# Optimization experiments

Hardware: AMD Instinct MI355X
Metric: run time of the kernel (lower is better)

The kernel has to match this reference:

```python
import jax, jax.numpy as jnp
import numpy as np

EPS = 1e-5

def _conv1x1(x, w):
    # x: (B, Cin, N, K), w: (Cout, Cin) -> (B, Cout, N, K)
    return jnp.einsum('oc,bcnk->bonk', w, x)

def _bn2d(x, gamma, beta):
    # eval-mode BN with running_mean=0, running_var=1 (fresh init)
    scale = gamma / jnp.sqrt(1.0 + EPS)
    return x * scale[None, :, None, None] + beta[None, :, None, None]

def setup_inputs() -> dict:
    key = jax.random.key(0)
    ks = jax.random.split(key, 10)
    B, Cin, N, K = 8, 64, 1024, 32
    Cout, M = 64, 8
    Cin2 = 2 * Cin  # kernel_input='w_neighbor'
    features = jax.random.normal(ks[0], (B, Cin, N, K), dtype=jnp.float32)
    points_xyz = jax.random.normal(ks[1], (B, 3, N, K), dtype=jnp.float32)
    # ScoreNet convs: mlp_channels [7,16,16,16,M]; first 3 have BN (no bias), last has bias
    w1 = jax.random.normal(ks[2], (16, 7), dtype=jnp.float32) * (2.0 / 7) ** 0.5
    w2 = jax.random.normal(ks[3], (16, 16), dtype=jnp.float32) * (2.0 / 16) ** 0.5
    w3 = jax.random.normal(ks[4], (16, 16), dtype=jnp.float32) * (2.0 / 16) ** 0.5
    w4 = jax.random.normal(ks[5], (M, 16), dtype=jnp.float32) * (2.0 / 16) ** 0.5
    b4 = jnp.zeros((M,), dtype=jnp.float32)
    g1 = jnp.ones((16,), jnp.float32); be1 = jnp.zeros((16,), jnp.float32)
    g2 = jnp.ones((16,), jnp.float32); be2 = jnp.zeros((16,), jnp.float32)
    g3 = jnp.ones((16,), jnp.float32); be3 = jnp.zeros((16,), jnp.float32)
    # weight bank: kaiming_normal on (M, 2Cin, Cout) -> stored as (2Cin, M, Cout)
    wb = jax.random.normal(ks[6], (Cin2, M, Cout), dtype=jnp.float32) * (2.0 / Cin2) ** 0.5
    bn_g = jnp.ones((Cout,), jnp.float32); bn_b = jnp.zeros((Cout,), jnp.float32)
    return dict(features=features, points_xyz=points_xyz,
                w1=w1, g1=g1, be1=be1, w2=w2, g2=g2, be2=be2,
                w3=w3, g3=g3, be3=be3, w4=w4, b4=b4,
                weight_bank=wb, bn_g=bn_g, bn_b=bn_b)

def reference(features, points_xyz, w1, g1, be1, w2, g2, be2, w3, g3, be3,
              w4, b4, weight_bank, bn_g, bn_b):
    B, Cin, N, K = features.shape
    M = weight_bank.shape[1]
    # kernel_input = 'w_neighbor': concat(feat - center, feat) -> (B, 2Cin, N, K)
    center_f = features[..., :1]
    feat = jnp.concatenate([features - center_f, features], axis=1)
    # scorenet input = 'w_neighbor_dist': (center_xyz, xyz_diff, dist) -> (B, 7, N, K)
    center_xyz = jnp.broadcast_to(points_xyz[..., :1], points_xyz.shape)
    xyz_diff = points_xyz - center_xyz
    dist = jnp.sqrt(jnp.sum(xyz_diff * xyz_diff, axis=1, keepdims=True))
    xyz_feats = jnp.concatenate([center_xyz, xyz_diff, dist], axis=1)
    h = jax.nn.relu(_bn2d(_conv1x1(xyz_feats, w1), g1, be1))
    h = jax.nn.relu(_bn2d(_conv1x1(h, w2), g2, be2))
    h = jax.nn.relu(_bn2d(_conv1x1(h, w3), g3, be3))
    s = _conv1x1(h, w4) + b4[None, :, None, None]  # (B, M, N, K)
    scores = jax.nn.softmax(s, axis=1)
    scores = jnp.transpose(scores, (0, 2, 3, 1))  # (B, N, K, M)
    # matmul with weight bank then score-weighted sum over kernels, fused via einsum
    # original: (B,N,K,2Cin)@(2Cin,M*Cout) -> (B,N,K,M,Cout); sum_m scores * . -> (B,N,K,Cout)
    new_features = jnp.einsum('bcnk,cmo,bnkm->bonk', feat, weight_bank, scores)
    # BN2d (eval, fresh stats) + ReLU
    new_features = jax.nn.relu(_bn2d(new_features, bn_g, bn_b))
    return new_features
```

## Files before the change

### kernel.cpp

```cpp
#include <hip/hip_runtime.h>
#include <hip/hip_bf16.h>

typedef _Float16 f16;
typedef __attribute__((ext_vector_type(2))) _Float16 f16x2;
typedef __attribute__((ext_vector_type(8))) _Float16 f16x8;
typedef __attribute__((ext_vector_type(16))) float f32x16;

#define BNSCL 0.9999950000375f

__global__ __launch_bounds__(256) void k_scores(
    const float* __restrict__ xyz,
    const float* __restrict__ w1, const float* __restrict__ g1, const float* __restrict__ be1,
    const float* __restrict__ w2, const float* __restrict__ g2, const float* __restrict__ be2,
    const float* __restrict__ w3, const float* __restrict__ g3, const float* __restrict__ be3,
    const float* __restrict__ w4, const float* __restrict__ b4,
    const float* __restrict__ wb, f16* __restrict__ wbtA,
    f16* __restrict__ scores)
{
    __shared__ float lw[856];
    const int tid = threadIdx.x;

    if (blockIdx.x < 256) {
        int idx = blockIdx.x * 256 + tid;
        int j    = idx & 7;
        int lane = (idx >> 3) & 63;
        int ks   = (idx >> 9) & 63;
        int ot   = idx >> 15;
        int cp   = ks * 2 + (lane >> 5);
        int o    = ot * 32 + (lane & 31);
        wbtA[idx] = (f16)wb[(cp * 8 + j) * 64 + o];
    }

    if (tid < 112) lw[tid] = w1[tid];
    lw[112 + tid] = w2[tid];
    lw[368 + tid] = w3[tid];
    if (tid < 128) lw[624 + tid] = w4[tid];
    if (tid < 8)   lw[752 + tid] = b4[tid];
    if (tid < 16) {
        lw[760 + tid] = g1[tid] * BNSCL;  lw[776 + tid] = be1[tid];
        lw[792 + tid] = g2[tid] * BNSCL;  lw[808 + tid] = be2[tid];
        lw[824 + tid] = g3[tid] * BNSCL;  lw[840 + tid] = be3[tid];
    }
    __syncthreads();

    float in7[2][7], h1[2][16], h2[2][16], s[2][8];

#pragma unroll
    for (int q = 0; q < 2; ++q) {
        int g = blockIdx.x * 512 + q * 256 + tid;
        int b = g >> 15;
        int p = g & 32767;
        int pc = p & ~31;
        const float* xb = xyz + (size_t)b * 98304;
        float cx = xb[pc], cy = xb[32768 + pc], cz = xb[65536 + pc];
        float dx = xb[p] - cx, dy = xb[32768 + p] - cy, dz = xb[65536 + p] - cz;
        in7[q][0] = cx; in7[q][1] = cy; in7[q][2] = cz;
        in7[q][3] = dx; in7[q][4] = dy; in7[q][5] = dz;
        in7[q][6] = sqrtf(dx * dx + dy * dy + dz * dz);
    }

#pragma unroll
    for (int o = 0; o < 16; ++o) {
        float a0 = 0.f, a1 = 0.f;
#pragma unroll
        for (int c = 0; c < 7; ++c) {
            float w = lw[o * 7 + c];
            a0 += w * in7[0][c]; a1 += w * in7[1][c];
        }
        float gs = lw[760 + o], bb = lw[776 + o];
        h1[0][o] = fmaxf(a0 * gs + bb, 0.f);
        h1[1][o] = fmaxf(a1 * gs + bb, 0.f);
    }
#pragma unroll
    for (int o = 0; o < 16; ++o) {
        float a0 = 0.f, a1 = 0.f;
#pragma unroll
        for (int c = 0; c < 16; ++c) {
            float w = lw[112 + o * 16 + c];
            a0 += w * h1[0][c]; a1 += w * h1[1][c];
        }
        float gs = lw[792 + o], bb = lw[808 + o];
        h2[0][o] = fmaxf(a0 * gs + bb, 0.f);
        h2[1][o] = fmaxf(a1 * gs + bb, 0.f);
    }
#pragma unroll
    for (int o = 0; o < 16; ++o) {
        float a0 = 0.f, a1 = 0.f;
#pragma unroll
        for (int c = 0; c < 16; ++c) {
            float w = lw[368 + o * 16 + c];
            a0 += w * h2[0][c]; a1 += w * h2[1][c];
        }
        float gs = lw[824 + o], bb = lw[840 + o];
        h1[0][o] = fmaxf(a0 * gs + bb, 0.f);
        h1[1][o] = fmaxf(a1 * gs + bb, 0.f);
    }
#pragma unroll
    for (int o = 0; o < 8; ++o) {
        float bb = lw[752 + o];
        float a0 = bb, a1 = bb;
#pragma unroll
        for (int c = 0; c < 16; ++c) {
            float w = lw[624 + o * 16 + c];
            a0 += w * h1[0][c]; a1 += w * h1[1][c];
        }
        s[0][o] = a0; s[1][o] = a1;
    }

#pragma unroll
    for (int q = 0; q < 2; ++q) {
        int g = blockIdx.x * 512 + q * 256 + tid;
        float mx = s[q][0];
#pragma unroll
        for (int i = 1; i < 8; ++i) mx = fmaxf(mx, s[q][i]);
        float sum = 0.f;
#pragma unroll
        for (int i = 0; i < 8; ++i) { s[q][i] = __expf(s[q][i] - mx); sum += s[q][i]; }
        float inv = 1.f / sum;
        f16x8 o8;
#pragma unroll
        for (int i = 0; i < 8; ++i) o8[i] = (f16)(s[q][i] * inv);
        *(f16x8*)(scores + (size_t)g * 8) = o8;
    }
}

__global__ __launch_bounds__(512, 4) void k_main(
    const float* __restrict__ feat,
    const f16* __restrict__ scores,
    const f16* __restrict__ wbtA,
    const float* __restrict__ bn_g, const float* __restrict__ bn_b,
    float* __restrict__ out)
{
    __shared__ __align__(16) f16 lwb[32768];

    const int tid  = threadIdx.x;
    const int lane = tid & 63;
    const int wave = tid >> 6;
    const int l31  = lane & 31;
    const int lh   = lane >> 5;

    const int ot = blockIdx.x >> 9;
    const int g  = blockIdx.x & 511;
    const int pblock = g * 512;
    const int b    = pblock >> 15;
    const int pt0  = (pblock & 32767) + wave * 64;
    const int pc0  = pt0 + l31;
    const int pc1  = pc0 + 32;

    const f16* src = wbtA + ((size_t)ot << 15);
#pragma unroll
    for (int it = 0; it < 8; ++it) {
        int idx = it * 512 + tid;
        *(int4*)&lwb[idx << 3] = *(const int4*)&src[idx << 3];
    }
    __syncthreads();

    const float* fb = feat + (size_t)b * 2097152;

    const int gpt = pblock + wave * 64 + l31;
    f16x8 sv0 = *(const f16x8*)(scores + (size_t)gpt * 8);
    f16x8 sv1 = *(const f16x8*)(scores + (size_t)(gpt + 32) * 8);
    const f16x2 s0a = {sv0[0], sv0[1]}, s0b = {sv0[2], sv0[3]},
                s0c = {sv0[4], sv0[5]}, s0d = {sv0[6], sv0[7]};
    const f16x2 s1a = {sv1[0], sv1[1]}, s1b = {sv1[2], sv1[3]},
                s1c = {sv1[4], sv1[5]}, s1d = {sv1[6], sv1[7]};

    f32x16 acc0 = {}, acc1 = {};

    const f16* Alds = lwb + (lane << 3);

#pragma unroll 2
    for (int kk = 0; kk < 32; ++kk) {
        const float* fr = fb + ((size_t)(kk * 2 + lh) << 15);

        f16x8 aD = *(const f16x8*)(Alds + ((size_t)kk << 9));
        f16x8 aR = *(const f16x8*)(Alds + ((size_t)(kk + 32) << 9));

        float fv0 = fr[pc0], fv1 = fr[pc1];
        float fc0 = fr[pt0], fc1 = fr[pt0 + 32];

        f16 hR0 = (f16)fv0,          hR1 = (f16)fv1;
        f16 hD0 = (f16)(fv0 - fc0),  hD1 = (f16)(fv1 - fc1);
        f16x2 fR0 = {hR0, hR0}, fR1 = {hR1, hR1};
        f16x2 fD0 = {hD0, hD0}, fD1 = {hD1, hD1};

        f16x2 d0a = fD0 * s0a, d0b = fD0 * s0b, d0c = fD0 * s0c, d0d = fD0 * s0d;
        f16x2 d1a = fD1 * s1a, d1b = fD1 * s1b, d1c = fD1 * s1c, d1d = fD1 * s1d;
        f16x2 r0a = fR0 * s0a, r0b = fR0 * s0b, r0c = fR0 * s0c, r0d = fR0 * s0d;
        f16x2 r1a = fR1 * s1a, r1b = fR1 * s1b, r1c = fR1 * s1c, r1d = fR1 * s1d;

        f16x8 bD0 = {d0a[0],d0a[1],d0b[0],d0b[1],d0c[0],d0c[1],d0d[0],d0d[1]};
        f16x8 bD1 = {d1a[0],d1a[1],d1b[0],d1b[1],d1c[0],d1c[1],d1d[0],d1d[1]};
        f16x8 bR0 = {r0a[0],r0a[1],r0b[0],r0b[1],r0c[0],r0c[1],r0d[0],r0d[1]};
        f16x8 bR1 = {r1a[0],r1a[1],r1b[0],r1b[1],r1c[0],r1c[1],r1d[0],r1d[1]};

        acc0 = __builtin_amdgcn_mfma_f32_32x32x16_f16(aD, bD0, acc0, 0, 0, 0);
        acc1 = __builtin_amdgcn_mfma_f32_32x32x16_f16(aD, bD1, acc1, 0, 0, 0);
        acc0 = __builtin_amdgcn_mfma_f32_32x32x16_f16(aR, bR0, acc0, 0, 0, 0);
        acc1 = __builtin_amdgcn_mfma_f32_32x32x16_f16(aR, bR1, acc1, 0, 0, 0);
    }

#pragma unroll
    for (int q = 0; q < 2; ++q) {
        int pcol = (q == 0) ? pc0 : pc1;
        const f32x16& a = (q == 0) ? acc0 : acc1;
#pragma unroll
        for (int r = 0; r < 16; ++r) {
            int o = ot * 32 + (r & 3) + ((r >> 2) << 3) + (lh << 2);
            float v = a[r];
            v = v * (bn_g[o] * BNSCL) + bn_b[o];
            v = fmaxf(v, 0.f);
            out[((size_t)(b * 64 + o) << 15) + pcol] = v;
        }
    }
}

extern "C" void kernel_launch(void* const* d_in, const int* in_sizes, int n_in,
                              void* d_out, int out_size, void* d_ws, size_t ws_size,
                              hipStream_t stream)
{
    const float* features = (const float*)d_in[0];
    const float* xyz      = (const float*)d_in[1];
    const float* w1  = (const float*)d_in[2];
    const float* g1  = (const float*)d_in[3];
    const float* be1 = (const float*)d_in[4];
    const float* w2  = (const float*)d_in[5];
    const float* g2  = (const float*)d_in[6];
    const float* be2 = (const float*)d_in[7];
    const float* w3  = (const float*)d_in[8];
    const float* g3  = (const float*)d_in[9];
    const float* be3 = (const float*)d_in[10];
    const float* w4  = (const float*)d_in[11];
    const float* b4  = (const float*)d_in[12];
    const float* wb  = (const float*)d_in[13];
    const float* bn_g = (const float*)d_in[14];
    const float* bn_b = (const float*)d_in[15];

    f16* scores = (f16*)d_ws;
    f16* wbtA   = (f16*)((char*)d_ws + (4u << 20));

    k_scores<<<512, 256, 0, stream>>>(xyz, w1, g1, be1, w2, g2, be2,
                                      w3, g3, be3, w4, b4, wb, wbtA, scores);
    k_main<<<1024, 512, 0, stream>>>(features, scores, wbtA, bn_g, bn_b,
                                     (float*)d_out);
}
```

Baseline: 180.7 us.

## Software-pipeline feature loads four steps ahead and overlap with LDS weight fill

Feature loads for the first four k-steps and the score loads are issued before the shared-memory weight copy and barrier, so global latency overlaps the LDS fill. The k-loop is fully unrolled with a 4-deep register ring that prefetches the features four steps ahead of their use in the MFMA chain. The epilogue is merged so each BN parameter is loaded once per row. This raises register pressure from the extra in-flight values and the full unroll, which could lower occupancy.

```diff
diff --git a/kernel.cpp b/kernel.cpp
--- a/kernel.cpp
+++ b/kernel.cpp
@@ -147,6 +147,20 @@
     const int pc0  = pt0 + l31;
     const int pc1  = pc0 + 32;
 
+    const float* fb  = feat + (size_t)b * 2097152;
+    const float* frb = fb + ((size_t)lh << 15);
+
+    float pA[4], pB[4], pC[4], pD[4];
+#pragma unroll
+    for (int d = 0; d < 4; ++d) {
+        const float* fr = frb + ((size_t)d << 16);
+        pA[d] = fr[pc0]; pB[d] = fr[pc1]; pC[d] = fr[pt0]; pD[d] = fr[pt0 + 32];
+    }
+
+    const int gpt = pblock + wave * 64 + l31;
+    f16x8 sv0 = *(const f16x8*)(scores + (size_t)gpt * 8);
+    f16x8 sv1 = *(const f16x8*)(scores + (size_t)(gpt + 32) * 8);
+
     const f16* src = wbtA + ((size_t)ot << 15);
 #pragma unroll
     for (int it = 0; it < 8; ++it) {
@@ -155,11 +169,6 @@
     }
     __syncthreads();
 
-    const float* fb = feat + (size_t)b * 2097152;
-
-    const int gpt = pblock + wave * 64 + l31;
-    f16x8 sv0 = *(const f16x8*)(scores + (size_t)gpt * 8);
-    f16x8 sv1 = *(const f16x8*)(scores + (size_t)(gpt + 32) * 8);
     const f16x2 s0a = {sv0[0], sv0[1]}, s0b = {sv0[2], sv0[3]},
                 s0c = {sv0[4], sv0[5]}, s0d = {sv0[6], sv0[7]};
     const f16x2 s1a = {sv1[0], sv1[1]}, s1b = {sv1[2], sv1[3]},
@@ -169,49 +178,48 @@
 
     const f16* Alds = lwb + (lane << 3);
 
-#pragma unroll 2
-    for (int kk = 0; kk < 32; ++kk) {
-        const float* fr = fb + ((size_t)(kk * 2 + lh) << 15);
-
-        f16x8 aD = *(const f16x8*)(Alds + ((size_t)kk << 9));
-        f16x8 aR = *(const f16x8*)(Alds + ((size_t)(kk + 32) << 9));
-
-        float fv0 = fr[pc0], fv1 = fr[pc1];
-        float fc0 = fr[pt0], fc1 = fr[pt0 + 32];
-
-        f16 hR0 = (f16)fv0,          hR1 = (f16)fv1;
-        f16 hD0 = (f16)(fv0 - fc0),  hD1 = (f16)(fv1 - fc1);
-        f16x2 fR0 = {hR0, hR0}, fR1 = {hR1, hR1};
-        f16x2 fD0 = {hD0, hD0}, fD1 = {hD1, hD1};
-
-        f16x2 d0a = fD0 * s0a, d0b = fD0 * s0b, d0c = fD0 * s0c, d0d = fD0 * s0d;
-        f16x2 d1a = fD1 * s1a, d1b = fD1 * s1b, d1c = fD1 * s1c, d1d = fD1 * s1d;
-        f16x2 r0a = fR0 * s0a, r0b = fR0 * s0b, r0c = fR0 * s0c, r0d = fR0 * s0d;
-        f16x2 r1a = fR1 * s1a, r1b = fR1 * s1b, r1c = fR1 * s1c, r1d = fR1 * s1d;
-
-        f16x8 bD0 = {d0a[0],d0a[1],d0b[0],d0b[1],d0c[0],d0c[1],d0d[0],d0d[1]};
-        f16x8 bD1 = {d1a[0],d1a[1],d1b[0],d1b[1],d1c[0],d1c[1],d1d[0],d1d[1]};
-        f16x8 bR0 = {r0a[0],r0a[1],r0b[0],r0b[1],r0c[0],r0c[1],r0d[0],r0d[1]};
-        f16x8 bR1 = {r1a[0],r1a[1],r1b[0],r1b[1],r1c[0],r1c[1],r1d[0],r1d[1]};
-
-        acc0 = __builtin_amdgcn_mfma_f32_32x32x16_f16(aD, bD0, acc0, 0, 0, 0);
-        acc1 = __builtin_amdgcn_mfma_f32_32x32x16_f16(aD, bD1, acc1, 0, 0, 0);
-        acc0 = __builtin_amdgcn_mfma_f32_32x32x16_f16(aR, bR0, acc0, 0, 0, 0);
-        acc1 = __builtin_amdgcn_mfma_f32_32x32x16_f16(aR, bR1, acc1, 0, 0, 0);
-    }
-
-#pragma unroll
-    for (int q = 0; q < 2; ++q) {
-        int pcol = (q == 0) ? pc0 : pc1;
-        const f32x16& a = (q == 0) ? acc0 : acc1;
-#pragma unroll
-        for (int r = 0; r < 16; ++r) {
-            int o = ot * 32 + (r & 3) + ((r >> 2) << 3) + (lh << 2);
-            float v = a[r];
-            v = v * (bn_g[o] * BNSCL) + bn_b[o];
-            v = fmaxf(v, 0.f);
-            out[((size_t)(b * 64 + o) << 15) + pcol] = v;
-        }
+#define KSTEP(kk, RELOAD)                                                      \
+    {                                                                          \
+        const int d_ = (kk) & 3;                                               \
+        float fv0 = pA[d_], fv1 = pB[d_], fc0 = pC[d_], fc1 = pD[d_];          \
+        if (RELOAD) {                                                          \
+            const float* fr_ = frb + ((size_t)((kk) + 4) << 16);               \
+            pA[d_] = fr_[pc0]; pB[d_] = fr_[pc1];                              \
+            pC[d_] = fr_[pt0]; pD[d_] = fr_[pt0 + 32];                         \
+        }                                                                      \
+        f16x8 aD = *(const f16x8*)(Alds + ((size_t)(kk) << 9));                \
+        f16x8 aR = *(const f16x8*)(Alds + ((size_t)((kk) + 32) << 9));         \
+        f16 hR0 = (f16)fv0,          hR1 = (f16)fv1;                           \
+        f16 hD0 = (f16)(fv0 - fc0),  hD1 = (f16)(fv1 - fc1);                   \
+        f16x2 fR0 = {hR0, hR0}, fR1 = {hR1, hR1};                              \
+        f16x2 fD0 = {hD0, hD0}, fD1 = {hD1, hD1};                              \
+        f16x2 d0a = fD0 * s0a, d0b = fD0 * s0b, d0c = fD0 * s0c, d0d = fD0 * s0d; \
+        f16x2 d1a = fD1 * s1a, d1b = fD1 * s1b, d1c = fD1 * s1c, d1d = fD1 * s1d; \
+        f16x2 r0a = fR0 * s0a, r0b = fR0 * s0b, r0c = fR0 * s0c, r0d = fR0 * s0d; \
+        f16x2 r1a = fR1 * s1a, r1b = fR1 * s1b, r1c = fR1 * s1c, r1d = fR1 * s1d; \
+        f16x8 bD0 = {d0a[0],d0a[1],d0b[0],d0b[1],d0c[0],d0c[1],d0d[0],d0d[1]}; \
+        f16x8 bD1 = {d1a[0],d1a[1],d1b[0],d1b[1],d1c[0],d1c[1],d1d[0],d1d[1]}; \
+        f16x8 bR0 = {r0a[0],r0a[1],r0b[0],r0b[1],r0c[0],r0c[1],r0d[0],r0d[1]}; \
+        f16x8 bR1 = {r1a[0],r1a[1],r1b[0],r1b[1],r1c[0],r1c[1],r1d[0],r1d[1]}; \
+        acc0 = __builtin_amdgcn_mfma_f32_32x32x16_f16(aD, bD0, acc0, 0, 0, 0); \
+        acc1 = __builtin_amdgcn_mfma_f32_32x32x16_f16(aD, bD1, acc1, 0, 0, 0); \
+        acc0 = __builtin_amdgcn_mfma_f32_32x32x16_f16(aR, bR0, acc0, 0, 0, 0); \
+        acc1 = __builtin_amdgcn_mfma_f32_32x32x16_f16(aR, bR1, acc1, 0, 0, 0); \
+    }
+
+#define KS4(b0, R) KSTEP(b0, R) KSTEP((b0)+1, R) KSTEP((b0)+2, R) KSTEP((b0)+3, R)
+    KS4(0, 1)  KS4(4, 1)  KS4(8, 1)  KS4(12, 1)
+    KS4(16, 1) KS4(20, 1) KS4(24, 1) KS4(28, 0)
+#undef KS4
+#undef KSTEP
+
+#pragma unroll
+    for (int r = 0; r < 16; ++r) {
+        int o = ot * 32 + (r & 3) + ((r >> 2) << 3) + (lh << 2);
+        float gs = bn_g[o] * BNSCL, bb = bn_b[o];
+        size_t row = (size_t)(b * 64 + o) << 15;
+        out[row + pc0] = fmaxf(acc0[r] * gs + bb, 0.f);
+        out[row + pc1] = fmaxf(acc1[r] * gs + bb, 0.f);
     }
 }
 
```

After: 182.0 us. No clear change (+0.8%).
